# Kernel optimization log

Hardware: AMD Instinct MI355X
Metric: run time of the kernel (lower is better)

## Reference

```python
import jax, jax.numpy as jnp
import numpy as np

B, HH, WW, C = 1, 96, 96, 128
HEADS, K = 4, 7

def setup_inputs() -> dict:
    key = jax.random.key(0)
    ks = jax.random.split(key, 6)
    def lin(k, o, i):
        return jax.random.normal(k, (o, i), jnp.float32) * (1.0 / np.sqrt(i))
    return {
        "x": jax.random.normal(ks[0], (B, HH, WW, C), jnp.float32),
        "qkv_w": lin(ks[1], 3 * C, C),
        "qkv_b": jnp.zeros((3 * C,), jnp.float32),
        "proj_w": lin(ks[2], C, C),
        "proj_b": jnp.zeros((C,), jnp.float32),
        "fc1_w": lin(ks[3], 4 * C, C),
        "fc1_b": jnp.zeros((4 * C,), jnp.float32),
        "fc2_w": lin(ks[4], C, 4 * C),
        "fc2_b": jnp.zeros((C,), jnp.float32),
    }

def _na2d(q, k, v):
    # q,k,v: [B, heads, H, W, hd]; NATTEN 2D neighborhood attention,
    # kernel K, stride 1, dilation 1, non-causal. Windows are clamped at
    # borders so each query attends to exactly K*K in-bounds keys.
    Bq, h, Hs, Ws, hd = q.shape
    start_h = jnp.clip(jnp.arange(Hs) - K // 2, 0, Hs - K)
    idx_h = start_h[:, None] + jnp.arange(K)  # [H, K]
    start_w = jnp.clip(jnp.arange(Ws) - K // 2, 0, Ws - K)
    idx_w = start_w[:, None] + jnp.arange(K)  # [W, K]
    I = idx_h[:, None, :, None]  # -> [H, W, K, K] broadcast
    J = idx_w[None, :, None, :]
    k_nb = k[:, :, I, J, :]  # [B, heads, H, W, K, K, hd]
    v_nb = v[:, :, I, J, :]
    scale = jnp.asarray(hd, q.dtype) ** -0.5
    logits = jnp.einsum('bhijd,bhijkld->bhijkl', q, k_nb) * scale
    attn = jax.nn.softmax(logits.reshape(Bq, h, Hs, Ws, K * K), axis=-1)
    attn = attn.reshape(Bq, h, Hs, Ws, K, K)
    return jnp.einsum('bhijkl,bhijkld->bhijd', attn, v_nb)

def reference(x, qkv_w, qkv_b, proj_w, proj_b, fc1_w, fc1_b, fc2_w, fc2_b):
    Bq, Hs, Ws, Cc = x.shape
    hd = Cc // HEADS
    qkv = x @ qkv_w.T + qkv_b  # [B,H,W,3C]
    q, k, v = jnp.split(qkv, 3, axis=-1)
    def to_heads(t):
        return t.reshape(Bq, Hs, Ws, HEADS, hd).transpose(0, 3, 1, 2, 4)
    o = _na2d(to_heads(q), to_heads(k), to_heads(v))  # [B,heads,H,W,hd]
    o = o.transpose(0, 2, 3, 1, 4).reshape(Bq, Hs, Ws, Cc)
    x0 = o @ proj_w.T + proj_b
    h1 = jax.nn.gelu(x0 @ fc1_w.T + fc1_b, approximate=False)
    return h1 @ fc2_w.T + fc2_b
```

## Files before the change

### kernel.cpp

```cpp
#include <hip/hip_runtime.h>

typedef __bf16 bf16_t;
typedef __bf16 bf16x8 __attribute__((ext_vector_type(8)));
typedef __bf16 bf16x4 __attribute__((ext_vector_type(4)));
typedef float f32x4 __attribute__((ext_vector_type(4)));
typedef int   i32x4 __attribute__((ext_vector_type(4)));

#define HH 96
#define WW 96
#define CC 128
#define HD 32
#define TOK (HH * WW)
#define PLANE (TOK * CC)
#define KW 7

#define W_QKV  0
#define W_PROJ 49152
#define W_FC1  65536
#define W_FC2  131072
#define W_TOT  196608

#define PATCH 10
#define PSZ 100
#define NPAD 112
#define STR 136
#define H1S 520

#define L_P    0
#define L_OS   8704
#define L_X0   10880
#define L_VOFF 13056
#define L_TOT  13312

template <int NT>
__device__ __forceinline__ void mmaN(const bf16_t* __restrict__ A, int lda,
                                     const bf16_t* __restrict__ W, int ldb,
                                     int K, f32x4* acc) {
    const int lane = threadIdx.x & 63;
    const bf16_t* ap = A + (lane & 15) * lda + ((lane >> 4) * 8);
    const bf16_t* bp = W + (lane & 15) * ldb + ((lane >> 4) * 8);
    for (int k0 = 0; k0 < K; k0 += 32) {
        bf16x8 a = *(const bf16x8*)(ap + k0);
#pragma unroll
        for (int t = 0; t < NT; t++) {
            bf16x8 b = *(const bf16x8*)(bp + t * 16 * ldb + k0);
            acc[t] = __builtin_amdgcn_mfma_f32_16x16x32_bf16(a, b, acc[t], 0, 0, 0);
        }
    }
}

__global__ __launch_bounds__(256) void k_prep(const float* __restrict__ x,
                                              const float* __restrict__ qkv_w,
                                              const float* __restrict__ proj_w,
                                              const float* __restrict__ fc1_w,
                                              const float* __restrict__ fc2_w,
                                              bf16_t* __restrict__ xb,
                                              bf16_t* __restrict__ wb) {
    const int idx = blockIdx.x * 256 + threadIdx.x;
    const int NX = PLANE / 4;
    const float* src;
    bf16_t* dst;
    int base;
    if (idx < NX) {
        base = idx * 4; src = x + base; dst = xb + base;
    } else {
        base = (idx - NX) * 4;
        if (base >= W_TOT) return;
        dst = wb + base;
        if (base < W_PROJ)     src = qkv_w  + base;
        else if (base < W_FC1) src = proj_w + (base - W_PROJ);
        else if (base < W_FC2) src = fc1_w  + (base - W_FC1);
        else                   src = fc2_w  + (base - W_FC2);
    }
    const f32x4 a = *(const f32x4*)src;
    bf16x4 r;
    r[0] = (bf16_t)a[0]; r[1] = (bf16_t)a[1]; r[2] = (bf16_t)a[2]; r[3] = (bf16_t)a[3];
    *(bf16x4*)dst = r;
}

__global__ __launch_bounds__(256) void k_qkv(const bf16_t* __restrict__ xb,
                                             const bf16_t* __restrict__ wb,
                                             const float* __restrict__ bias,
                                             bf16_t* __restrict__ qb,
                                             bf16_t* __restrict__ kb,
                                             bf16_t* __restrict__ vb) {
    const int wid = blockIdx.x * 4 + (threadIdx.x >> 6);
    const int m0 = (wid / 6) * 16;
    const int n0 = (wid % 6) * 64;
    const int lane = threadIdx.x & 63;
    const int g = lane >> 4, li = lane & 15;
    f32x4 acc[4] = {};
    mmaN<4>(xb + m0 * CC, CC, wb + W_QKV + n0 * CC, CC, CC, acc);
#pragma unroll
    for (int t = 0; t < 4; t++) {
        const int n = n0 + t * 16 + li;
        const float bb = bias[n];
        const int part = n >> 7, c = n & 127;
        bf16_t* dst = (part == 0) ? qb : (part == 1) ? kb : vb;
#pragma unroll
        for (int r = 0; r < 4; r++)
            dst[(m0 + g * 4 + r) * CC + c] = (bf16_t)(acc[t][r] + bb);
    }
}

__global__ __launch_bounds__(256, 3) void k_attn_mlp(
        const bf16_t* __restrict__ qb, const bf16_t* __restrict__ kg,
        const bf16_t* __restrict__ vg, const bf16_t* __restrict__ wb,
        const float* __restrict__ proj_b, const float* __restrict__ fc1_b,
        const float* __restrict__ fc2_b,  float* __restrict__ out) {
    __shared__ __align__(16) bf16_t smem[L_TOT];
    bf16_t* Pbuf = smem + L_P;
    bf16_t* o_s  = smem + L_OS;
    bf16_t* x0s  = smem + L_X0;
    bf16_t* h1s  = smem + L_P;
    int*    voff = (int*)(smem + L_VOFF);

    const int tid = threadIdx.x;
    const int w = tid >> 6, lane = tid & 63;
    const int g = lane >> 4, li = lane & 15;
    const int bid = (blockIdx.x & 7) * 72 + (blockIdx.x >> 3);
    const int i0 = (bid / 24) * 4, j0 = (bid % 24) * 4;
    const int pr0 = min(max(i0 - 3, 0), HH - PATCH);
    const int pc0 = min(max(j0 - 3, 0), WW - PATCH);
    const int ch = w * HD;

    if (tid < 128) {
        const int p = min(tid, PSZ - 1);
        const int pi = p / 10, pj = p - 10 * pi;
        voff[tid] = ((pr0 + pi) * WW + pc0 + pj) * CC;
    }
    __syncthreads();

    f32x4 lg[7];
    {
        const int qi = i0 + (li >> 2), qj = j0 + (li & 3);
        const bf16x8 aq = *(const bf16x8*)(qb + (qi * WW + qj) * CC + ch + g * 8);
#pragma unroll
        for (int t = 0; t < 7; t++) {
            const bf16x8 bk = *(const bf16x8*)(kg + voff[t * 16 + li] + ch + g * 8);
            lg[t] = __builtin_amdgcn_mfma_f32_16x16x32_bf16(aq, bk, (f32x4){0.f,0.f,0.f,0.f}, 0, 0, 0);
        }
    }
    int lr[4], lc[4];
#pragma unroll
    for (int r = 0; r < 4; r++) {
        const int m = g * 4 + r;
        const int i = i0 + (m >> 2), j = j0 + (m & 3);
        lr[r] = min(max(i - 3, 0), HH - KW) - pr0;
        lc[r] = min(max(j - 3, 0), WW - KW) - pc0;
    }
    const float scale = 0.17677669529663687f;
#pragma unroll
    for (int t = 0; t < 7; t++) {
        const int col = t * 16 + li;
        const int pi = col / 10, pj = col - 10 * pi;
#pragma unroll
        for (int r = 0; r < 4; r++) {
            const bool valid = (col < PSZ) &&
                               ((unsigned)(pi - lr[r]) <= 6u) &&
                               ((unsigned)(pj - lc[r]) <= 6u);
            lg[t][r] = valid ? lg[t][r] * scale : -1e30f;
        }
    }
    f32x4 mx = lg[0], sm;
#pragma unroll
    for (int t = 1; t < 7; t++)
#pragma unroll
        for (int r = 0; r < 4; r++) mx[r] = fmaxf(mx[r], lg[t][r]);
#pragma unroll
    for (int off = 8; off; off >>= 1)
#pragma unroll
        for (int r = 0; r < 4; r++) mx[r] = fmaxf(mx[r], __shfl_xor(mx[r], off));
#pragma unroll
    for (int r = 0; r < 4; r++) sm[r] = 0.f;
#pragma unroll
    for (int t = 0; t < 7; t++)
#pragma unroll
        for (int r = 0; r < 4; r++) {
            lg[t][r] = __expf(lg[t][r] - mx[r]);
            sm[r] += lg[t][r];
        }
#pragma unroll
    for (int off = 8; off; off >>= 1)
#pragma unroll
        for (int r = 0; r < 4; r++) sm[r] += __shfl_xor(sm[r], off);
#pragma unroll
    for (int r = 0; r < 4; r++) sm[r] = 1.f / sm[r];

    bf16_t* Pw = Pbuf + w * 16 * STR;
#pragma unroll
    for (int t = 0; t < 7; t++)
#pragma unroll
        for (int r = 0; r < 4; r++)
            Pw[(g * 4 + r) * STR + t * 16 + li] = (bf16_t)(lg[t][r] * sm[r]);
    *(bf16x4*)(Pw + (lane >> 2) * STR + NPAD + (lane & 3) * 4) = (bf16x4){0,0,0,0};

    f32x4 oA[2] = {};
#pragma unroll
    for (int ks0 = 0; ks0 < 128; ks0 += 32) {
        const bf16x8 a = *(const bf16x8*)(Pw + li * STR + ks0 + g * 8);
        const i32x4 o0 = *(const i32x4*)&voff[ks0 + g * 8];
        const i32x4 o1 = *(const i32x4*)&voff[ks0 + g * 8 + 4];
#pragma unroll
        for (int t2 = 0; t2 < 2; t2++) {
            const int cb = ch + t2 * 16 + li;
            bf16x8 b;
            b[0] = vg[o0[0] + cb]; b[1] = vg[o0[1] + cb];
            b[2] = vg[o0[2] + cb]; b[3] = vg[o0[3] + cb];
            b[4] = vg[o1[0] + cb]; b[5] = vg[o1[1] + cb];
            b[6] = vg[o1[2] + cb]; b[7] = vg[o1[3] + cb];
            oA[t2] = __builtin_amdgcn_mfma_f32_16x16x32_bf16(a, b, oA[t2], 0, 0, 0);
        }
    }
#pragma unroll
    for (int t2 = 0; t2 < 2; t2++)
#pragma unroll
        for (int r = 0; r < 4; r++)
            o_s[(g * 4 + r) * STR + ch + t2 * 16 + li] = (bf16_t)oA[t2][r];
    __syncthreads();

    {
        f32x4 acc[2] = {};
        mmaN<2>(o_s, STR, wb + W_PROJ + (w * 32) * CC, CC, CC, acc);
#pragma unroll
        for (int t = 0; t < 2; t++) {
            const int n = w * 32 + t * 16 + li;
            const float bb = proj_b[n];
#pragma unroll
            for (int r = 0; r < 4; r++)
                x0s[(g * 4 + r) * STR + n] = (bf16_t)(acc[t][r] + bb);
        }
    }
    __syncthreads();

    {
        f32x4 acc[8] = {};
        mmaN<8>(x0s, STR, wb + W_FC1 + (w * 128) * CC, CC, CC, acc);
#pragma unroll
        for (int t = 0; t < 8; t++) {
            const int n = w * 128 + t * 16 + li;
            const float bb = fc1_b[n];
#pragma unroll
            for (int r = 0; r < 4; r++) {
                const int m = g * 4 + r;
                const float xv = acc[t][r] + bb;
                const float u = 0.7978845608028654f * (xv + 0.044715f * xv * xv * xv);
                const float e = __expf(2.f * u);
                const float gg = 0.5f * xv * (2.f - 2.f / (e + 1.f));
                h1s[m * H1S + n] = (bf16_t)gg;
            }
        }
    }
    __syncthreads();

    {
        f32x4 acc[2] = {};
        mmaN<2>(h1s, H1S, wb + W_FC2 + (w * 32) * (4 * CC), 4 * CC, 4 * CC, acc);
#pragma unroll
        for (int t = 0; t < 2; t++) {
            const int n = w * 32 + t * 16 + li;
            const float bb = fc2_b[n];
#pragma unroll
            for (int r = 0; r < 4; r++) {
                const int m = g * 4 + r;
                const int i = i0 + (m >> 2), j = j0 + (m & 3);
                float xv = acc[t][r] + bb;
                xv = fminf(fmaxf(xv, -1e4f), 1e4f);
                out[(i * WW + j) * CC + n] = xv;
            }
        }
    }
}

extern "C" void kernel_launch(void* const* d_in, const int* in_sizes, int n_in,
                              void* d_out, int out_size, void* d_ws, size_t ws_size,
                              hipStream_t stream) {
    const float* x      = (const float*)d_in[0];
    const float* qkv_w  = (const float*)d_in[1];
    const float* qkv_b  = (const float*)d_in[2];
    const float* proj_w = (const float*)d_in[3];
    const float* proj_b = (const float*)d_in[4];
    const float* fc1_w  = (const float*)d_in[5];
    const float* fc1_b  = (const float*)d_in[6];
    const float* fc2_w  = (const float*)d_in[7];
    const float* fc2_b  = (const float*)d_in[8];

    bf16_t* ws = (bf16_t*)d_ws;
    bf16_t* wb = ws;
    bf16_t* xb = ws + W_TOT;
    bf16_t* qb = xb + PLANE;
    bf16_t* kb = qb + PLANE;
    bf16_t* vb = kb + PLANE;
    float* out = (float*)d_out;

    k_prep<<<1344, 256, 0, stream>>>(x, qkv_w, proj_w, fc1_w, fc2_w, xb, wb);
    k_qkv <<<864,  256, 0, stream>>>(xb, wb, qkv_b, qb, kb, vb);
    k_attn_mlp<<<576, 256, 0, stream>>>(qb, kb, vb, wb, proj_b, fc1_b, fc2_b, out);
}
```

Baseline: 118.2 us.

## Stage transposed V patch in shared memory for vectorized PV loads

Each block now loads its 10x10 V patch once with coalesced 16-byte global reads and writes it transposed into LDS. The PV MFMA then reads its B operand as a single bf16x8 LDS load instead of eight scattered 2-byte global gathers. The voff offset table is dropped and K addresses are computed inline. In exchange, LDS use per block grows from about 26KB to about 48KB, which may limit how many blocks fit per CU. It also adds a scalar transpose-store loop with likely bank conflicts and an extra barrier.

```diff
diff --git a/kernel.cpp b/kernel.cpp
--- a/kernel.cpp
+++ b/kernel.cpp
@@ -4,7 +4,6 @@
 typedef __bf16 bf16x8 __attribute__((ext_vector_type(8)));
 typedef __bf16 bf16x4 __attribute__((ext_vector_type(4)));
 typedef float f32x4 __attribute__((ext_vector_type(4)));
-typedef int   i32x4 __attribute__((ext_vector_type(4)));
 
 #define HH 96
 #define WW 96
@@ -25,12 +24,13 @@
 #define NPAD 112
 #define STR 136
 #define H1S 520
+#define VSTR 120
 
 #define L_P    0
+#define L_VT   8704
 #define L_OS   8704
 #define L_X0   10880
-#define L_VOFF 13056
-#define L_TOT  13312
+#define L_TOT  24064
 
 template <int NT>
 __device__ __forceinline__ void mmaN(const bf16_t* __restrict__ A, int lda,
@@ -110,10 +110,10 @@
         const float* __restrict__ fc2_b,  float* __restrict__ out) {
     __shared__ __align__(16) bf16_t smem[L_TOT];
     bf16_t* Pbuf = smem + L_P;
+    bf16_t* Vt   = smem + L_VT;
     bf16_t* o_s  = smem + L_OS;
     bf16_t* x0s  = smem + L_X0;
     bf16_t* h1s  = smem + L_P;
-    int*    voff = (int*)(smem + L_VOFF);
 
     const int tid = threadIdx.x;
     const int w = tid >> 6, lane = tid & 63;
@@ -124,12 +124,18 @@
     const int pc0 = min(max(j0 - 3, 0), WW - PATCH);
     const int ch = w * HD;
 
-    if (tid < 128) {
-        const int p = min(tid, PSZ - 1);
-        const int pi = p / 10, pj = p - 10 * pi;
-        voff[tid] = ((pr0 + pi) * WW + pc0 + pj) * CC;
-    }
-    __syncthreads();
+    bf16x8 vs[8];
+    const int sp = tid >> 1;
+    const int sh = (tid & 1) * 64;
+    if (sp < PSZ) {
+        const int spi = sp / 10, spj = sp - 10 * spi;
+        const bf16_t* vsrc = vg + ((pr0 + spi) * WW + pc0 + spj) * CC + sh;
+#pragma unroll
+        for (int j = 0; j < 8; j++) vs[j] = *(const bf16x8*)(vsrc + j * 8);
+    } else {
+#pragma unroll
+        for (int j = 0; j < 8; j++) vs[j] = (bf16x8){0, 0, 0, 0, 0, 0, 0, 0};
+    }
 
     f32x4 lg[7];
     {
@@ -137,10 +143,24 @@
         const bf16x8 aq = *(const bf16x8*)(qb + (qi * WW + qj) * CC + ch + g * 8);
 #pragma unroll
         for (int t = 0; t < 7; t++) {
-            const bf16x8 bk = *(const bf16x8*)(kg + voff[t * 16 + li] + ch + g * 8);
+            const int col = t * 16 + li;
+            const int p = min(col, PSZ - 1);
+            const int pi2 = p / 10, pj2 = p - 10 * pi2;
+            const bf16x8 bk = *(const bf16x8*)(kg +
+                ((pr0 + pi2) * WW + pc0 + pj2) * CC + ch + g * 8);
             lg[t] = __builtin_amdgcn_mfma_f32_16x16x32_bf16(aq, bk, (f32x4){0.f,0.f,0.f,0.f}, 0, 0, 0);
         }
     }
+
+    if (sp < 112) {
+        bf16_t* vt = Vt + sp;
+#pragma unroll
+        for (int j = 0; j < 8; j++)
+#pragma unroll
+            for (int e = 0; e < 8; e++)
+                vt[(sh + j * 8 + e) * VSTR] = vs[j][e];
+    }
+
     int lr[4], lc[4];
 #pragma unroll
     for (int r = 0; r < 4; r++) {
@@ -195,23 +215,21 @@
             Pw[(g * 4 + r) * STR + t * 16 + li] = (bf16_t)(lg[t][r] * sm[r]);
     *(bf16x4*)(Pw + (lane >> 2) * STR + NPAD + (lane & 3) * 4) = (bf16x4){0,0,0,0};
 
+    __syncthreads();
+
     f32x4 oA[2] = {};
 #pragma unroll
     for (int ks0 = 0; ks0 < 128; ks0 += 32) {
         const bf16x8 a = *(const bf16x8*)(Pw + li * STR + ks0 + g * 8);
-        const i32x4 o0 = *(const i32x4*)&voff[ks0 + g * 8];
-        const i32x4 o1 = *(const i32x4*)&voff[ks0 + g * 8 + 4];
+        const int pcol = min(ks0 + g * 8, 104);
 #pragma unroll
         for (int t2 = 0; t2 < 2; t2++) {
             const int cb = ch + t2 * 16 + li;
-            bf16x8 b;
-            b[0] = vg[o0[0] + cb]; b[1] = vg[o0[1] + cb];
-            b[2] = vg[o0[2] + cb]; b[3] = vg[o0[3] + cb];
-            b[4] = vg[o1[0] + cb]; b[5] = vg[o1[1] + cb];
-            b[6] = vg[o1[2] + cb]; b[7] = vg[o1[3] + cb];
+            const bf16x8 b = *(const bf16x8*)(Vt + cb * VSTR + pcol);
             oA[t2] = __builtin_amdgcn_mfma_f32_16x16x32_bf16(a, b, oA[t2], 0, 0, 0);
         }
     }
+    __syncthreads();
 #pragma unroll
     for (int t2 = 0; t2 < 2; t2++)
 #pragma unroll
```

After: 119.5 us. No clear change (+1.1%).

## Prefetch V gathers and next-stage weight fragments before barriers in fused block kernel

Applied to the files above, without the earlier changes.

Issues the scattered V gathers into registers before the QK logits and softmax, and loads the proj, fc1 and fc2 weight fragments for the next stage before each barrier, so global latency overlaps with current compute. It also replaces __syncthreads with a custom barrier that waits only on LDS counters (lgkmcnt) and not on outstanding global loads. This raises register pressure (V fragments and weight fragments held across stages), which could lower occupancy.

```diff
diff --git a/kernel.cpp b/kernel.cpp
--- a/kernel.cpp
+++ b/kernel.cpp
@@ -31,6 +31,8 @@
 #define L_X0   10880
 #define L_VOFF 13056
 #define L_TOT  13312
+
+#define BAR() asm volatile("s_waitcnt lgkmcnt(0)\n\ts_barrier" ::: "memory")
 
 template <int NT>
 __device__ __forceinline__ void mmaN(const bf16_t* __restrict__ A, int lda,
@@ -40,6 +42,29 @@
     const bf16_t* ap = A + (lane & 15) * lda + ((lane >> 4) * 8);
     const bf16_t* bp = W + (lane & 15) * ldb + ((lane >> 4) * 8);
     for (int k0 = 0; k0 < K; k0 += 32) {
+        bf16x8 a = *(const bf16x8*)(ap + k0);
+#pragma unroll
+        for (int t = 0; t < NT; t++) {
+            bf16x8 b = *(const bf16x8*)(bp + t * 16 * ldb + k0);
+            acc[t] = __builtin_amdgcn_mfma_f32_16x16x32_bf16(a, b, acc[t], 0, 0, 0);
+        }
+    }
+}
+
+template <int NT>
+__device__ __forceinline__ void mmaN_pre(const bf16_t* __restrict__ A, int lda,
+                                         const bf16_t* __restrict__ W, int ldb,
+                                         int K, f32x4* acc, const bf16x8* b0) {
+    const int lane = threadIdx.x & 63;
+    const bf16_t* ap = A + (lane & 15) * lda + ((lane >> 4) * 8);
+    const bf16_t* bp = W + (lane & 15) * ldb + ((lane >> 4) * 8);
+    {
+        bf16x8 a = *(const bf16x8*)ap;
+#pragma unroll
+        for (int t = 0; t < NT; t++)
+            acc[t] = __builtin_amdgcn_mfma_f32_16x16x32_bf16(a, b0[t], acc[t], 0, 0, 0);
+    }
+    for (int k0 = 32; k0 < K; k0 += 32) {
         bf16x8 a = *(const bf16x8*)(ap + k0);
 #pragma unroll
         for (int t = 0; t < NT; t++) {
@@ -129,78 +154,13 @@
         const int pi = p / 10, pj = p - 10 * pi;
         voff[tid] = ((pr0 + pi) * WW + pc0 + pj) * CC;
     }
-    __syncthreads();
-
-    f32x4 lg[7];
-    {
-        const int qi = i0 + (li >> 2), qj = j0 + (li & 3);
-        const bf16x8 aq = *(const bf16x8*)(qb + (qi * WW + qj) * CC + ch + g * 8);
-#pragma unroll
-        for (int t = 0; t < 7; t++) {
-            const bf16x8 bk = *(const bf16x8*)(kg + voff[t * 16 + li] + ch + g * 8);
-            lg[t] = __builtin_amdgcn_mfma_f32_16x16x32_bf16(aq, bk, (f32x4){0.f,0.f,0.f,0.f}, 0, 0, 0);
-        }
-    }
-    int lr[4], lc[4];
-#pragma unroll
-    for (int r = 0; r < 4; r++) {
-        const int m = g * 4 + r;
-        const int i = i0 + (m >> 2), j = j0 + (m & 3);
-        lr[r] = min(max(i - 3, 0), HH - KW) - pr0;
-        lc[r] = min(max(j - 3, 0), WW - KW) - pc0;
-    }
-    const float scale = 0.17677669529663687f;
-#pragma unroll
-    for (int t = 0; t < 7; t++) {
-        const int col = t * 16 + li;
-        const int pi = col / 10, pj = col - 10 * pi;
-#pragma unroll
-        for (int r = 0; r < 4; r++) {
-            const bool valid = (col < PSZ) &&
-                               ((unsigned)(pi - lr[r]) <= 6u) &&
-                               ((unsigned)(pj - lc[r]) <= 6u);
-            lg[t][r] = valid ? lg[t][r] * scale : -1e30f;
-        }
-    }
-    f32x4 mx = lg[0], sm;
-#pragma unroll
-    for (int t = 1; t < 7; t++)
-#pragma unroll
-        for (int r = 0; r < 4; r++) mx[r] = fmaxf(mx[r], lg[t][r]);
-#pragma unroll
-    for (int off = 8; off; off >>= 1)
-#pragma unroll
-        for (int r = 0; r < 4; r++) mx[r] = fmaxf(mx[r], __shfl_xor(mx[r], off));
-#pragma unroll
-    for (int r = 0; r < 4; r++) sm[r] = 0.f;
-#pragma unroll
-    for (int t = 0; t < 7; t++)
-#pragma unroll
-        for (int r = 0; r < 4; r++) {
-            lg[t][r] = __expf(lg[t][r] - mx[r]);
-            sm[r] += lg[t][r];
-        }
-#pragma unroll
-    for (int off = 8; off; off >>= 1)
-#pragma unroll
-        for (int r = 0; r < 4; r++) sm[r] += __shfl_xor(sm[r], off);
-#pragma unroll
-    for (int r = 0; r < 4; r++) sm[r] = 1.f / sm[r];
-
-    bf16_t* Pw = Pbuf + w * 16 * STR;
-#pragma unroll
-    for (int t = 0; t < 7; t++)
-#pragma unroll
-        for (int r = 0; r < 4; r++)
-            Pw[(g * 4 + r) * STR + t * 16 + li] = (bf16_t)(lg[t][r] * sm[r]);
-    *(bf16x4*)(Pw + (lane >> 2) * STR + NPAD + (lane & 3) * 4) = (bf16x4){0,0,0,0};
-
-    f32x4 oA[2] = {};
-#pragma unroll
-    for (int ks0 = 0; ks0 < 128; ks0 += 32) {
-        const bf16x8 a = *(const bf16x8*)(Pw + li * STR + ks0 + g * 8);
-        const i32x4 o0 = *(const i32x4*)&voff[ks0 + g * 8];
-        const i32x4 o1 = *(const i32x4*)&voff[ks0 + g * 8 + 4];
+    BAR();
+
+    bf16x8 vf[4][2];
+#pragma unroll
+    for (int kk = 0; kk < 4; kk++) {
+        const i32x4 o0 = *(const i32x4*)&voff[kk * 32 + g * 8];
+        const i32x4 o1 = *(const i32x4*)&voff[kk * 32 + g * 8 + 4];
 #pragma unroll
         for (int t2 = 0; t2 < 2; t2++) {
             const int cb = ch + t2 * 16 + li;
@@ -209,19 +169,114 @@
             b[2] = vg[o0[2] + cb]; b[3] = vg[o0[3] + cb];
             b[4] = vg[o1[0] + cb]; b[5] = vg[o1[1] + cb];
             b[6] = vg[o1[2] + cb]; b[7] = vg[o1[3] + cb];
-            oA[t2] = __builtin_amdgcn_mfma_f32_16x16x32_bf16(a, b, oA[t2], 0, 0, 0);
-        }
+            vf[kk][t2] = b;
+        }
+    }
+
+    f32x4 lg[7];
+    {
+        const int qi = i0 + (li >> 2), qj = j0 + (li & 3);
+        const bf16x8 aq = *(const bf16x8*)(qb + (qi * WW + qj) * CC + ch + g * 8);
+#pragma unroll
+        for (int t = 0; t < 7; t++) {
+            const bf16x8 bk = *(const bf16x8*)(kg + voff[t * 16 + li] + ch + g * 8);
+            lg[t] = __builtin_amdgcn_mfma_f32_16x16x32_bf16(aq, bk, (f32x4){0.f,0.f,0.f,0.f}, 0, 0, 0);
+        }
+    }
+    int lr[4], lc[4];
+#pragma unroll
+    for (int r = 0; r < 4; r++) {
+        const int m = g * 4 + r;
+        const int i = i0 + (m >> 2), j = j0 + (m & 3);
+        lr[r] = min(max(i - 3, 0), HH - KW) - pr0;
+        lc[r] = min(max(j - 3, 0), WW - KW) - pc0;
+    }
+    const float scale = 0.17677669529663687f;
+#pragma unroll
+    for (int t = 0; t < 7; t++) {
+        const int col = t * 16 + li;
+        const int pi = col / 10, pj = col - 10 * pi;
+#pragma unroll
+        for (int r = 0; r < 4; r++) {
+            const bool valid = (col < PSZ) &&
+                               ((unsigned)(pi - lr[r]) <= 6u) &&
+                               ((unsigned)(pj - lc[r]) <= 6u);
+            lg[t][r] = valid ? lg[t][r] * scale : -1e30f;
+        }
+    }
+    f32x4 mx = lg[0], sm;
+#pragma unroll
+    for (int t = 1; t < 7; t++)
+#pragma unroll
+        for (int r = 0; r < 4; r++) mx[r] = fmaxf(mx[r], lg[t][r]);
+#pragma unroll
+    for (int off = 8; off; off >>= 1)
+#pragma unroll
+        for (int r = 0; r < 4; r++) mx[r] = fmaxf(mx[r], __shfl_xor(mx[r], off));
+#pragma unroll
+    for (int r = 0; r < 4; r++) sm[r] = 0.f;
+#pragma unroll
+    for (int t = 0; t < 7; t++)
+#pragma unroll
+        for (int r = 0; r < 4; r++) {
+            lg[t][r] = __expf(lg[t][r] - mx[r]);
+            sm[r] += lg[t][r];
+        }
+#pragma unroll
+    for (int off = 8; off; off >>= 1)
+#pragma unroll
+        for (int r = 0; r < 4; r++) sm[r] += __shfl_xor(sm[r], off);
+#pragma unroll
+    for (int r = 0; r < 4; r++) sm[r] = 1.f / sm[r];
+
+    bf16_t* Pw = Pbuf + w * 16 * STR;
+#pragma unroll
+    for (int t = 0; t < 7; t++)
+#pragma unroll
+        for (int r = 0; r < 4; r++)
+            Pw[(g * 4 + r) * STR + t * 16 + li] = (bf16_t)(lg[t][r] * sm[r]);
+    *(bf16x4*)(Pw + (lane >> 2) * STR + NPAD + (lane & 3) * 4) = (bf16x4){0,0,0,0};
+
+    f32x4 oA[2] = {};
+#pragma unroll
+    for (int kk = 0; kk < 4; kk++) {
+        const bf16x8 a = *(const bf16x8*)(Pw + li * STR + kk * 32 + g * 8);
+#pragma unroll
+        for (int t2 = 0; t2 < 2; t2++)
+            oA[t2] = __builtin_amdgcn_mfma_f32_16x16x32_bf16(a, vf[kk][t2], oA[t2], 0, 0, 0);
+    }
+
+    bf16x8 pjb[4][2];
+    {
+        const bf16_t* pw = wb + W_PROJ + (w * 32 + li) * CC + g * 8;
+#pragma unroll
+        for (int kk = 0; kk < 4; kk++)
+#pragma unroll
+            for (int t = 0; t < 2; t++)
+                pjb[kk][t] = *(const bf16x8*)(pw + t * 16 * CC + kk * 32);
     }
 #pragma unroll
     for (int t2 = 0; t2 < 2; t2++)
 #pragma unroll
         for (int r = 0; r < 4; r++)
             o_s[(g * 4 + r) * STR + ch + t2 * 16 + li] = (bf16_t)oA[t2][r];
-    __syncthreads();
+    BAR();
 
     {
         f32x4 acc[2] = {};
-        mmaN<2>(o_s, STR, wb + W_PROJ + (w * 32) * CC, CC, CC, acc);
+        const bf16_t* ap = o_s + li * STR + g * 8;
+#pragma unroll
+        for (int kk = 0; kk < 4; kk++) {
+            const bf16x8 a = *(const bf16x8*)(ap + kk * 32);
+            acc[0] = __builtin_amdgcn_mfma_f32_16x16x32_bf16(a, pjb[kk][0], acc[0], 0, 0, 0);
+            acc[1] = __builtin_amdgcn_mfma_f32_16x16x32_bf16(a, pjb[kk][1], acc[1], 0, 0, 0);
+        }
+        bf16x8 f1b[8];
+        {
+            const bf16_t* fw = wb + W_FC1 + (w * 128 + li) * CC + g * 8;
+#pragma unroll
+            for (int t = 0; t < 8; t++) f1b[t] = *(const bf16x8*)(fw + t * 16 * CC);
+        }
 #pragma unroll
         for (int t = 0; t < 2; t++) {
             const int n = w * 32 + t * 16 + li;
@@ -230,12 +285,16 @@
             for (int r = 0; r < 4; r++)
                 x0s[(g * 4 + r) * STR + n] = (bf16_t)(acc[t][r] + bb);
         }
-    }
-    __syncthreads();
-
-    {
-        f32x4 acc[8] = {};
-        mmaN<8>(x0s, STR, wb + W_FC1 + (w * 128) * CC, CC, CC, acc);
+        BAR();
+
+        f32x4 acc1[8] = {};
+        mmaN_pre<8>(x0s, STR, wb + W_FC1 + (w * 128) * CC, CC, CC, acc1, f1b);
+        bf16x8 f2b[2];
+        {
+            const bf16_t* fw = wb + W_FC2 + (w * 32 + li) * (4 * CC) + g * 8;
+            f2b[0] = *(const bf16x8*)fw;
+            f2b[1] = *(const bf16x8*)(fw + 16 * 4 * CC);
+        }
 #pragma unroll
         for (int t = 0; t < 8; t++) {
             const int n = w * 128 + t * 16 + li;
@@ -243,19 +302,17 @@
 #pragma unroll
             for (int r = 0; r < 4; r++) {
                 const int m = g * 4 + r;
-                const float xv = acc[t][r] + bb;
+                const float xv = acc1[t][r] + bb;
                 const float u = 0.7978845608028654f * (xv + 0.044715f * xv * xv * xv);
                 const float e = __expf(2.f * u);
                 const float gg = 0.5f * xv * (2.f - 2.f / (e + 1.f));
                 h1s[m * H1S + n] = (bf16_t)gg;
             }
         }
-    }
-    __syncthreads();
-
-    {
-        f32x4 acc[2] = {};
-        mmaN<2>(h1s, H1S, wb + W_FC2 + (w * 32) * (4 * CC), 4 * CC, 4 * CC, acc);
+        BAR();
+
+        f32x4 acc2[2] = {};
+        mmaN_pre<2>(h1s, H1S, wb + W_FC2 + (w * 32) * (4 * CC), 4 * CC, 4 * CC, acc2, f2b);
 #pragma unroll
         for (int t = 0; t < 2; t++) {
             const int n = w * 32 + t * 16 + li;
@@ -264,7 +321,7 @@
             for (int r = 0; r < 4; r++) {
                 const int m = g * 4 + r;
                 const int i = i0 + (m >> 2), j = j0 + (m & 3);
-                float xv = acc[t][r] + bb;
+                float xv = acc2[t][r] + bb;
                 xv = fminf(fmaxf(xv, -1e4f), 1e4f);
                 out[(i * WW + j) * CC + n] = xv;
             }
```

Result: no change. 118.0 us (-0.1%).

## Halve attention tile to 2x4 queries, prefetch V before QK, lighter barriers

Applied to the files above, without the earlier changes.

Each block now handles a 2x4 query tile with an 8x10 key/value patch instead of 4x4 with 10x10, doubling the grid to 1152 blocks. The tile rows are duplicated to fill the 16-row MFMA, and the extra rows are dropped when writing the output. V gathers are issued into registers before the QK logits so their latency overlaps the softmax. __syncthreads is replaced by an LDS-only waitcnt plus s_barrier, and occupancy is raised to 4 blocks per SM. The cost is that half the MLP MFMA work is spent on duplicated rows and the proj/fc1/fc2 weights are read by twice as many blocks.

```diff
diff --git a/kernel.cpp b/kernel.cpp
--- a/kernel.cpp
+++ b/kernel.cpp
@@ -20,17 +20,21 @@
 #define W_FC2  131072
 #define W_TOT  196608
 
-#define PATCH 10
-#define PSZ 100
-#define NPAD 112
+#define PR 8
+#define PCW 10
+#define PSZ 80
+#define PVK 96
+#define PSTR 104
 #define STR 136
 #define H1S 520
 
 #define L_P    0
-#define L_OS   8704
-#define L_X0   10880
-#define L_VOFF 13056
-#define L_TOT  13312
+#define L_OS   8320
+#define L_X0   10496
+#define L_VOFF 12672
+#define L_TOT  12864
+
+#define BAR() asm volatile("s_waitcnt lgkmcnt(0)\n\ts_barrier" ::: "memory")
 
 template <int NT>
 __device__ __forceinline__ void mmaN(const bf16_t* __restrict__ A, int lda,
@@ -103,7 +107,7 @@
     }
 }
 
-__global__ __launch_bounds__(256, 3) void k_attn_mlp(
+__global__ __launch_bounds__(256, 4) void k_attn_mlp(
         const bf16_t* __restrict__ qb, const bf16_t* __restrict__ kg,
         const bf16_t* __restrict__ vg, const bf16_t* __restrict__ wb,
         const float* __restrict__ proj_b, const float* __restrict__ fc1_b,
@@ -118,89 +122,24 @@
     const int tid = threadIdx.x;
     const int w = tid >> 6, lane = tid & 63;
     const int g = lane >> 4, li = lane & 15;
-    const int bid = (blockIdx.x & 7) * 72 + (blockIdx.x >> 3);
-    const int i0 = (bid / 24) * 4, j0 = (bid % 24) * 4;
-    const int pr0 = min(max(i0 - 3, 0), HH - PATCH);
-    const int pc0 = min(max(j0 - 3, 0), WW - PATCH);
+    const int bid = (blockIdx.x & 7) * 144 + (blockIdx.x >> 3);
+    const int i0 = (bid / 24) * 2, j0 = (bid % 24) * 4;
+    const int pr0 = min(max(i0 - 3, 0), HH - PR);
+    const int pc0 = min(max(j0 - 3, 0), WW - PCW);
     const int ch = w * HD;
 
-    if (tid < 128) {
+    if (tid < PVK) {
         const int p = min(tid, PSZ - 1);
         const int pi = p / 10, pj = p - 10 * pi;
         voff[tid] = ((pr0 + pi) * WW + pc0 + pj) * CC;
     }
-    __syncthreads();
-
-    f32x4 lg[7];
-    {
-        const int qi = i0 + (li >> 2), qj = j0 + (li & 3);
-        const bf16x8 aq = *(const bf16x8*)(qb + (qi * WW + qj) * CC + ch + g * 8);
-#pragma unroll
-        for (int t = 0; t < 7; t++) {
-            const bf16x8 bk = *(const bf16x8*)(kg + voff[t * 16 + li] + ch + g * 8);
-            lg[t] = __builtin_amdgcn_mfma_f32_16x16x32_bf16(aq, bk, (f32x4){0.f,0.f,0.f,0.f}, 0, 0, 0);
-        }
-    }
-    int lr[4], lc[4];
-#pragma unroll
-    for (int r = 0; r < 4; r++) {
-        const int m = g * 4 + r;
-        const int i = i0 + (m >> 2), j = j0 + (m & 3);
-        lr[r] = min(max(i - 3, 0), HH - KW) - pr0;
-        lc[r] = min(max(j - 3, 0), WW - KW) - pc0;
-    }
-    const float scale = 0.17677669529663687f;
-#pragma unroll
-    for (int t = 0; t < 7; t++) {
-        const int col = t * 16 + li;
-        const int pi = col / 10, pj = col - 10 * pi;
-#pragma unroll
-        for (int r = 0; r < 4; r++) {
-            const bool valid = (col < PSZ) &&
-                               ((unsigned)(pi - lr[r]) <= 6u) &&
-                               ((unsigned)(pj - lc[r]) <= 6u);
-            lg[t][r] = valid ? lg[t][r] * scale : -1e30f;
-        }
-    }
-    f32x4 mx = lg[0], sm;
-#pragma unroll
-    for (int t = 1; t < 7; t++)
-#pragma unroll
-        for (int r = 0; r < 4; r++) mx[r] = fmaxf(mx[r], lg[t][r]);
-#pragma unroll
-    for (int off = 8; off; off >>= 1)
-#pragma unroll
-        for (int r = 0; r < 4; r++) mx[r] = fmaxf(mx[r], __shfl_xor(mx[r], off));
-#pragma unroll
-    for (int r = 0; r < 4; r++) sm[r] = 0.f;
-#pragma unroll
-    for (int t = 0; t < 7; t++)
-#pragma unroll
-        for (int r = 0; r < 4; r++) {
-            lg[t][r] = __expf(lg[t][r] - mx[r]);
-            sm[r] += lg[t][r];
-        }
-#pragma unroll
-    for (int off = 8; off; off >>= 1)
-#pragma unroll
-        for (int r = 0; r < 4; r++) sm[r] += __shfl_xor(sm[r], off);
-#pragma unroll
-    for (int r = 0; r < 4; r++) sm[r] = 1.f / sm[r];
-
-    bf16_t* Pw = Pbuf + w * 16 * STR;
-#pragma unroll
-    for (int t = 0; t < 7; t++)
-#pragma unroll
-        for (int r = 0; r < 4; r++)
-            Pw[(g * 4 + r) * STR + t * 16 + li] = (bf16_t)(lg[t][r] * sm[r]);
-    *(bf16x4*)(Pw + (lane >> 2) * STR + NPAD + (lane & 3) * 4) = (bf16x4){0,0,0,0};
-
-    f32x4 oA[2] = {};
-#pragma unroll
-    for (int ks0 = 0; ks0 < 128; ks0 += 32) {
-        const bf16x8 a = *(const bf16x8*)(Pw + li * STR + ks0 + g * 8);
-        const i32x4 o0 = *(const i32x4*)&voff[ks0 + g * 8];
-        const i32x4 o1 = *(const i32x4*)&voff[ks0 + g * 8 + 4];
+    BAR();
+
+    bf16x8 vf[3][2];
+#pragma unroll
+    for (int kk = 0; kk < 3; kk++) {
+        const i32x4 o0 = *(const i32x4*)&voff[kk * 32 + g * 8];
+        const i32x4 o1 = *(const i32x4*)&voff[kk * 32 + g * 8 + 4];
 #pragma unroll
         for (int t2 = 0; t2 < 2; t2++) {
             const int cb = ch + t2 * 16 + li;
@@ -209,15 +148,88 @@
             b[2] = vg[o0[2] + cb]; b[3] = vg[o0[3] + cb];
             b[4] = vg[o1[0] + cb]; b[5] = vg[o1[1] + cb];
             b[6] = vg[o1[2] + cb]; b[7] = vg[o1[3] + cb];
-            oA[t2] = __builtin_amdgcn_mfma_f32_16x16x32_bf16(a, b, oA[t2], 0, 0, 0);
-        }
+            vf[kk][t2] = b;
+        }
+    }
+
+    f32x4 lg[5];
+    {
+        const int mm = li & 7;
+        const int qi = i0 + (mm >> 2), qj = j0 + (mm & 3);
+        const bf16x8 aq = *(const bf16x8*)(qb + (qi * WW + qj) * CC + ch + g * 8);
+#pragma unroll
+        for (int t = 0; t < 5; t++) {
+            const bf16x8 bk = *(const bf16x8*)(kg + voff[t * 16 + li] + ch + g * 8);
+            lg[t] = __builtin_amdgcn_mfma_f32_16x16x32_bf16(aq, bk, (f32x4){0.f,0.f,0.f,0.f}, 0, 0, 0);
+        }
+    }
+    int lr[4], lc[4];
+#pragma unroll
+    for (int r = 0; r < 4; r++) {
+        const int mm = (g * 4 + r) & 7;
+        const int i = i0 + (mm >> 2), j = j0 + (mm & 3);
+        lr[r] = min(max(i - 3, 0), HH - KW) - pr0;
+        lc[r] = min(max(j - 3, 0), WW - KW) - pc0;
+    }
+    const float scale = 0.17677669529663687f;
+#pragma unroll
+    for (int t = 0; t < 5; t++) {
+        const int col = t * 16 + li;
+        const int pi = col / 10, pj = col - 10 * pi;
+#pragma unroll
+        for (int r = 0; r < 4; r++) {
+            const bool valid = ((unsigned)(pi - lr[r]) <= 6u) &&
+                               ((unsigned)(pj - lc[r]) <= 6u);
+            lg[t][r] = valid ? lg[t][r] * scale : -1e30f;
+        }
+    }
+    f32x4 mx = lg[0], sm;
+#pragma unroll
+    for (int t = 1; t < 5; t++)
+#pragma unroll
+        for (int r = 0; r < 4; r++) mx[r] = fmaxf(mx[r], lg[t][r]);
+#pragma unroll
+    for (int off = 8; off; off >>= 1)
+#pragma unroll
+        for (int r = 0; r < 4; r++) mx[r] = fmaxf(mx[r], __shfl_xor(mx[r], off));
+#pragma unroll
+    for (int r = 0; r < 4; r++) sm[r] = 0.f;
+#pragma unroll
+    for (int t = 0; t < 5; t++)
+#pragma unroll
+        for (int r = 0; r < 4; r++) {
+            lg[t][r] = __expf(lg[t][r] - mx[r]);
+            sm[r] += lg[t][r];
+        }
+#pragma unroll
+    for (int off = 8; off; off >>= 1)
+#pragma unroll
+        for (int r = 0; r < 4; r++) sm[r] += __shfl_xor(sm[r], off);
+#pragma unroll
+    for (int r = 0; r < 4; r++) sm[r] = 1.f / sm[r];
+
+    bf16_t* Pw = Pbuf + w * 16 * PSTR;
+#pragma unroll
+    for (int t = 0; t < 5; t++)
+#pragma unroll
+        for (int r = 0; r < 4; r++)
+            Pw[(g * 4 + r) * PSTR + t * 16 + li] = (bf16_t)(lg[t][r] * sm[r]);
+    *(bf16x4*)(Pw + (lane >> 2) * PSTR + PSZ + (lane & 3) * 4) = (bf16x4){0,0,0,0};
+
+    f32x4 oA[2] = {};
+#pragma unroll
+    for (int kk = 0; kk < 3; kk++) {
+        const bf16x8 a = *(const bf16x8*)(Pw + li * PSTR + kk * 32 + g * 8);
+#pragma unroll
+        for (int t2 = 0; t2 < 2; t2++)
+            oA[t2] = __builtin_amdgcn_mfma_f32_16x16x32_bf16(a, vf[kk][t2], oA[t2], 0, 0, 0);
     }
 #pragma unroll
     for (int t2 = 0; t2 < 2; t2++)
 #pragma unroll
         for (int r = 0; r < 4; r++)
             o_s[(g * 4 + r) * STR + ch + t2 * 16 + li] = (bf16_t)oA[t2][r];
-    __syncthreads();
+    BAR();
 
     {
         f32x4 acc[2] = {};
@@ -231,7 +243,7 @@
                 x0s[(g * 4 + r) * STR + n] = (bf16_t)(acc[t][r] + bb);
         }
     }
-    __syncthreads();
+    BAR();
 
     {
         f32x4 acc[8] = {};
@@ -251,7 +263,7 @@
             }
         }
     }
-    __syncthreads();
+    BAR();
 
     {
         f32x4 acc[2] = {};
@@ -263,10 +275,12 @@
 #pragma unroll
             for (int r = 0; r < 4; r++) {
                 const int m = g * 4 + r;
-                const int i = i0 + (m >> 2), j = j0 + (m & 3);
-                float xv = acc[t][r] + bb;
-                xv = fminf(fmaxf(xv, -1e4f), 1e4f);
-                out[(i * WW + j) * CC + n] = xv;
+                if (m < 8) {
+                    const int i = i0 + (m >> 2), j = j0 + (m & 3);
+                    float xv = acc[t][r] + bb;
+                    xv = fminf(fmaxf(xv, -1e4f), 1e4f);
+                    out[(i * WW + j) * CC + n] = xv;
+                }
             }
         }
     }
@@ -295,5 +309,5 @@
 
     k_prep<<<1344, 256, 0, stream>>>(x, qkv_w, proj_w, fc1_w, fc2_w, xb, wb);
     k_qkv <<<864,  256, 0, stream>>>(xb, wb, qkv_b, qb, kb, vb);
-    k_attn_mlp<<<576, 256, 0, stream>>>(qb, kb, vb, wb, proj_b, fc1_b, fc2_b, out);
-}
+    k_attn_mlp<<<1152, 256, 0, stream>>>(qb, kb, vb, wb, proj_b, fc1_b, fc2_b, out);
+}
```

Measured after the change: 144.7 us. 22.4% more time.
